# Kernel optimization log

Hardware: AMD Instinct MI355X
Metric: run time of the kernel (lower is better)

Reference implementation:

```python
import jax, jax.numpy as jnp
import numpy as np

N_NODES = 100000
N_EDGES = 600000
HIDDEN = 128
BN_EPS = 1e-5


def setup_inputs() -> dict:
    key = jax.random.key(0)
    k_x, k_e, k_w, k_b, k_g = jax.random.split(key, 5)
    x = jax.random.normal(k_x, (N_NODES, HIDDEN), dtype=jnp.float32)
    edge_index = jax.random.randint(k_e, (2, N_EDGES), 0, N_NODES, dtype=jnp.int64)
    # GCNConv linear weight (no bias on the linear; bias added post-aggregation)
    scale = 1.0 / np.sqrt(HIDDEN)
    W = jax.random.uniform(k_w, (HIDDEN, HIDDEN), jnp.float32, -scale, scale)
    b = jax.random.uniform(k_b, (HIDDEN,), jnp.float32, -scale, scale)
    gamma = jnp.ones((HIDDEN,), jnp.float32)   # BatchNorm weight
    beta = jnp.zeros((HIDDEN,), jnp.float32)   # BatchNorm bias
    return {"x": x, "edge_index": edge_index, "W": W, "b": b, "gamma": gamma, "beta": beta}


def reference(x, edge_index, W, b, gamma, beta):
    N = x.shape[0]
    # ReLU then GCNConv linear transform: [N, D]
    h = jnp.matmul(jax.nn.relu(x), W)
    # Add self-loops (PyG GCNConv default)
    loops = jnp.arange(N, dtype=edge_index.dtype)
    row = jnp.concatenate([edge_index[0], loops])  # source nodes
    col = jnp.concatenate([edge_index[1], loops])  # target nodes
    # Symmetric normalization deg^{-1/2} with unit edge weights
    ones = jnp.ones(row.shape[0], dtype=h.dtype)
    deg = jax.ops.segment_sum(ones, col, num_segments=N)
    dinv = jnp.where(deg > 0, jax.lax.rsqrt(deg), 0.0)
    norm = dinv[row] * dinv[col]  # [E+N]
    # Gather -> scale -> scatter-add aggregation, then conv bias
    agg = jax.ops.segment_sum(norm[:, None] * h[row], col, num_segments=N)
    out = agg + b
    # BatchNorm1d (training mode: batch stats, biased variance)
    mean = jnp.mean(out, axis=0)
    var = jnp.var(out, axis=0)
    return gamma * (out - mean) * jax.lax.rsqrt(var + BN_EPS) + beta
```

## Files before the change

kernel.cpp:

```cpp
#include <hip/hip_runtime.h>

#define D 128
#define CAP 32
#define BN_EPS 1e-5f

typedef float floatx4 __attribute__((ext_vector_type(4)));
typedef __bf16 bf16x8 __attribute__((ext_vector_type(8)));

__device__ inline unsigned short f2bf(float f) {
    unsigned u; __builtin_memcpy(&u, &f, 4);
    unsigned r = (u + 0x7FFFu + ((u >> 16) & 1u)) >> 16;
    return (unsigned short)r;
}
__device__ inline float bflo(unsigned v) { unsigned x = v << 16; float f; __builtin_memcpy(&f, &x, 4); return f; }
__device__ inline float bfhi(unsigned v) { unsigned x = v & 0xFFFF0000u; float f; __builtin_memcpy(&f, &x, 4); return f; }

__global__ void setup_k(const unsigned* __restrict__ e, int* __restrict__ flag,
                        int* __restrict__ cursor, float* __restrict__ sums,
                        float* __restrict__ sumsq, const float* __restrict__ W,
                        unsigned short* __restrict__ Wt, int n_nodes) {
    int i = blockIdx.x * blockDim.x + threadIdx.x;
    if (i < n_nodes) cursor[i] = 0;
    if (i < D) { sums[i] = 0.f; sumsq[i] = 0.f; }
    if (i < D * D) {
        int n = i >> 7, k = i & 127;
        Wt[n * D + k] = f2bf(W[k * D + n]);
    }
    if (i == 0) {
        unsigned acc = 0;
        for (int k = 0; k < 64; ++k) acc |= e[2 * k + 1];
        *flag = (acc == 0u) ? 1 : 0;
    }
}

__global__ __launch_bounds__(256, 2) void gb_k(const float* __restrict__ x,
                                               const unsigned short* __restrict__ Wt,
                                               unsigned short* __restrict__ h,
                                               int n_mtiles,
                                               const void* __restrict__ ep,
                                               const int* __restrict__ flag,
                                               int* __restrict__ cursor,
                                               int* __restrict__ bucket,
                                               int n_edges) {
    int b = blockIdx.x;
    int g = b >> 3;
    int ngroups = (int)gridDim.x >> 3;
    int nbg = ngroups >> 2;

    if ((g & 3) == 3) {
        int bb = (g >> 2) * 8 + (b & 7);
        int stride = nbg * 8 * 256;
        int fl = *flag;
        for (int e = bb * 256 + (int)threadIdx.x; e < n_edges; e += stride) {
            int r, c;
            if (fl) {
                const long long* p = (const long long*)ep;
                r = (int)p[e]; c = (int)p[e + n_edges];
            } else {
                const int* p = (const int*)ep;
                r = p[e]; c = p[e + n_edges];
            }
            int pos = atomicAdd(&cursor[c], 1);
            if (pos < CAP) bucket[(size_t)c * CAP + pos] = r;
        }
        return;
    }

    int gg = (g >> 2) * 3 + (g & 3);
    int gb = gg * 8 + (b & 7);
    int lane = threadIdx.x & 63;
    int wave = gb * 4 + (threadIdx.x >> 6);
    int nw = (ngroups - nbg) * 32;
    int l15 = lane & 15;
    int quad = lane >> 4;

    bf16x8 Bf[4][8];
    for (int ks = 0; ks < 4; ++ks)
        for (int j = 0; j < 8; ++j)
            Bf[ks][j] = *(const bf16x8*)(Wt + (size_t)(j * 16 + l15) * D + ks * 32 + quad * 8);

    for (int mt = wave; mt < n_mtiles; mt += nw) {
        const float* xrow = x + (size_t)(mt * 16 + l15) * D + quad * 8;
        bf16x8 Af[4];
        for (int ks = 0; ks < 4; ++ks) {
            float4 a0 = *(const float4*)(xrow + ks * 32);
            float4 a1 = *(const float4*)(xrow + ks * 32 + 4);
            float av[8] = {a0.x, a0.y, a0.z, a0.w, a1.x, a1.y, a1.z, a1.w};
            union { unsigned short u[8]; bf16x8 v; } tmp;
            for (int jj = 0; jj < 8; ++jj) tmp.u[jj] = f2bf(fmaxf(av[jj], 0.0f));
            Af[ks] = tmp.v;
        }
        floatx4 acc[8];
        for (int j = 0; j < 8; ++j) acc[j] = (floatx4){0.f, 0.f, 0.f, 0.f};
        for (int ks = 0; ks < 4; ++ks)
            for (int j = 0; j < 8; ++j)
                acc[j] = __builtin_amdgcn_mfma_f32_16x16x32_bf16(Af[ks], Bf[ks][j], acc[j], 0, 0, 0);
        for (int j = 0; j < 8; ++j)
            for (int reg = 0; reg < 4; ++reg) {
                int rr = mt * 16 + quad * 4 + reg;
                int cc = j * 16 + l15;
                h[(size_t)rr * D + cc] = f2bf(acc[j][reg]);
            }
    }
}

__global__ void dinv_k(const int* __restrict__ cursor, float* __restrict__ dinv, int n_nodes) {
    int i = blockIdx.x * blockDim.x + threadIdx.x;
    if (i < n_nodes) dinv[i] = rsqrtf(1.0f + (float)cursor[i]);
}

#define PREPD(s, rr) { int r_ = ((s) < degc) ? (rr) : node;              \
                       w##s = ((s) < degc) ? dinv[r_] : 0.0f;            \
                       hv##s = hp[(unsigned)r_ * 64u + lane]; }
#define ACC(s) { ax += w##s * bflo(hv##s); ay += w##s * bfhi(hv##s); }

__global__ __launch_bounds__(256) void agg_k(const unsigned short* __restrict__ h,
                                             const int* __restrict__ bucket,
                                             const int* __restrict__ cursor,
                                             const float* __restrict__ dinv,
                                             unsigned* __restrict__ aggb,
                                             int n_nodes) {
    int lane = threadIdx.x & 63;
    int node = blockIdx.x * 4 + (threadIdx.x >> 6);
    if (node >= n_nodes) return;
    const unsigned* hp = (const unsigned*)h;

    int deg = cursor[node];
    int degc = deg < CAP ? deg : CAP;
    float dc = dinv[node];

    unsigned v = hp[(unsigned)node * 64u + lane];
    float ax = dc * bflo(v), ay = dc * bfhi(v);
    const int* bk = bucket + (size_t)node * CAP;

    float w0=0,w1=0,w2=0,w3=0,w4=0,w5=0,w6=0,w7=0;
    unsigned hv0=0,hv1=0,hv2=0,hv3=0,hv4=0,hv5=0,hv6=0,hv7=0;

    if (degc > 0) { int4 b = *(const int4*)(bk);     PREPD(0,b.x) PREPD(1,b.y) PREPD(2,b.z) PREPD(3,b.w) }
    if (degc > 4) { int4 b = *(const int4*)(bk + 4); PREPD(4,b.x) PREPD(5,b.y) PREPD(6,b.z) PREPD(7,b.w) }

    if (degc <= 8) {
        ACC(0) ACC(1) ACC(2) ACC(3) ACC(4) ACC(5) ACC(6) ACC(7)
    } else {
        float w8=0,w9=0,w10=0,w11=0,w12=0,w13=0,w14=0,w15=0;
        unsigned hv8=0,hv9=0,hv10=0,hv11=0,hv12=0,hv13=0,hv14=0,hv15=0;
        { int4 b = *(const int4*)(bk + 8); PREPD(8,b.x) PREPD(9,b.y) PREPD(10,b.z) PREPD(11,b.w) }
        if (degc > 12) { int4 b = *(const int4*)(bk + 12); PREPD(12,b.x) PREPD(13,b.y) PREPD(14,b.z) PREPD(15,b.w) }
        ACC(0)  ACC(1)  ACC(2)  ACC(3)  ACC(4)  ACC(5)  ACC(6)  ACC(7)
        ACC(8)  ACC(9)  ACC(10) ACC(11) ACC(12) ACC(13) ACC(14) ACC(15)
        for (int e = 16; e < degc; ++e) {
            int r = bk[e];
            float dr = dinv[r];
            unsigned hh = hp[(unsigned)r * 64u + lane];
            ax += dr * bflo(hh); ay += dr * bfhi(hh);
        }
    }

    float ox = dc * ax, oy = dc * ay;
    aggb[(unsigned)node * 64u + lane] = ((unsigned)f2bf(oy) << 16) | (unsigned)f2bf(ox);
}

__global__ __launch_bounds__(256) void stats_k(const unsigned* __restrict__ aggb,
                                               float* __restrict__ sums, float* __restrict__ sumsq,
                                               int n_nodes) {
    __shared__ float red[256];
    int lane = threadIdx.x & 63;
    int wib = threadIdx.x >> 6;
    int wave = blockIdx.x * 4 + wib;
    int nw = gridDim.x * 4;
    float s0 = 0.f, s1 = 0.f, q0 = 0.f, q1 = 0.f;
    int n = wave;
    for (; n + 3 * nw < n_nodes; n += 4 * nw) {
        unsigned p0 = aggb[(size_t)n * 64 + lane];
        unsigned p1 = aggb[(size_t)(n + nw) * 64 + lane];
        unsigned p2 = aggb[(size_t)(n + 2 * nw) * 64 + lane];
        unsigned p3 = aggb[(size_t)(n + 3 * nw) * 64 + lane];
        float a0 = bflo(p0), b0 = bfhi(p0), a1 = bflo(p1), b1 = bfhi(p1);
        float a2 = bflo(p2), b2 = bfhi(p2), a3 = bflo(p3), b3 = bfhi(p3);
        s0 += a0 + a1 + a2 + a3;
        s1 += b0 + b1 + b2 + b3;
        q0 += a0 * a0 + a1 * a1 + a2 * a2 + a3 * a3;
        q1 += b0 * b0 + b1 * b1 + b2 * b2 + b3 * b3;
    }
    for (; n < n_nodes; n += nw) {
        unsigned p = aggb[(size_t)n * 64 + lane];
        float vx = bflo(p), vy = bfhi(p);
        s0 += vx; s1 += vy; q0 += vx * vx; q1 += vy * vy;
    }
    red[threadIdx.x] = s0; __syncthreads();
    if (wib == 0) atomicAdd(&sums[2 * lane], red[lane] + red[64 + lane] + red[128 + lane] + red[192 + lane]);
    __syncthreads();
    red[threadIdx.x] = s1; __syncthreads();
    if (wib == 0) atomicAdd(&sums[2 * lane + 1], red[lane] + red[64 + lane] + red[128 + lane] + red[192 + lane]);
    __syncthreads();
    red[threadIdx.x] = q0; __syncthreads();
    if (wib == 0) atomicAdd(&sumsq[2 * lane], red[lane] + red[64 + lane] + red[128 + lane] + red[192 + lane]);
    __syncthreads();
    red[threadIdx.x] = q1; __syncthreads();
    if (wib == 0) atomicAdd(&sumsq[2 * lane + 1], red[lane] + red[64 + lane] + red[128 + lane] + red[192 + lane]);
}

__global__ __launch_bounds__(256) void final_k(const unsigned* __restrict__ aggb,
                                               const float* __restrict__ sums, const float* __restrict__ sumsq,
                                               const float* __restrict__ gamma, const float* __restrict__ beta,
                                               float* __restrict__ out, int total4, float inv_n) {
    int i = blockIdx.x * blockDim.x + threadIdx.x;
    if (i >= total4) return;
    int idx = i * 4;
    int f = idx & (D - 1);
    float4 sm = *(const float4*)(sums + f);
    float4 sq = *(const float4*)(sumsq + f);
    float4 g  = *(const float4*)(gamma + f);
    float4 bt = *(const float4*)(beta + f);
    uint2 p = *(const uint2*)(aggb + i * 2);

    float m0 = sm.x * inv_n, m1 = sm.y * inv_n, m2 = sm.z * inv_n, m3 = sm.w * inv_n;
    float sc0 = g.x * rsqrtf(sq.x * inv_n - m0 * m0 + BN_EPS);
    float sc1 = g.y * rsqrtf(sq.y * inv_n - m1 * m1 + BN_EPS);
    float sc2 = g.z * rsqrtf(sq.z * inv_n - m2 * m2 + BN_EPS);
    float sc3 = g.w * rsqrtf(sq.w * inv_n - m3 * m3 + BN_EPS);
    float4 o;
    o.x = fmaf(bflo(p.x), sc0, bt.x - m0 * sc0);
    o.y = fmaf(bfhi(p.x), sc1, bt.y - m1 * sc1);
    o.z = fmaf(bflo(p.y), sc2, bt.z - m2 * sc2);
    o.w = fmaf(bfhi(p.y), sc3, bt.w - m3 * sc3);
    *(float4*)(out + idx) = o;
}

extern "C" void kernel_launch(void* const* d_in, const int* in_sizes, int n_in,
                              void* d_out, int out_size, void* d_ws, size_t ws_size,
                              hipStream_t stream) {
    const float* x     = (const float*)d_in[0];
    const void*  edges = d_in[1];
    const float* W     = (const float*)d_in[2];
    const float* gamma = (const float*)d_in[4];
    const float* beta  = (const float*)d_in[5];
    float* out = (float*)d_out;

    int N = in_sizes[0] / D;
    int E = in_sizes[1] / 2;

    char* ws = (char*)d_ws;
    size_t off = 0;
    auto alloc = [&](size_t bytes) { void* p = ws + off; off += (bytes + 255) & ~(size_t)255; return p; };
    unsigned short* h  = (unsigned short*)alloc((size_t)N * D * 2);
    unsigned* aggb     = (unsigned*)alloc((size_t)N * D * 2);
    int* bucket        = (int*)alloc((size_t)N * CAP * 4);
    int* cursor        = (int*)alloc((size_t)N * 4);
    float* dinv        = (float*)alloc((size_t)N * 4);
    unsigned short* Wt = (unsigned short*)alloc((size_t)D * D * 2);
    float* sums        = (float*)alloc(512);
    float* sumsq       = (float*)alloc(512);
    int* flag          = (int*)alloc(16);

    int nblk = (N + 255) / 256;
    int n_mtiles = N / 16;

    setup_k<<<nblk, 256, 0, stream>>>((const unsigned*)edges, flag, cursor, sums, sumsq, W, Wt, N);
    gb_k<<<2080, 256, 0, stream>>>(x, Wt, h, n_mtiles, edges, flag, cursor, bucket, E);
    dinv_k<<<nblk, 256, 0, stream>>>(cursor, dinv, N);
    agg_k<<<(N + 3) / 4, 256, 0, stream>>>(h, bucket, cursor, dinv, aggb, N);
    stats_k<<<512, 256, 0, stream>>>(aggb, sums, sumsq, N);
    final_k<<<(N * D / 4 + 255) / 256, 256, 0, stream>>>(aggb, sums, sumsq, gamma, beta, out, N * D / 4, 1.0f / (float)N);
}
```

Measured before the change: 230.2 us.

## Co-schedule bucketing wave inside every GEMM block with unrolled batched atomics

Instead of assigning one quarter of the block groups to edge bucketing, each block now devotes one of its four waves (rotating by block index) to bucketing while the other three do the bf16 MFMA GEMM. The bucketing loop is unrolled twelve-fold, issuing all loads, then all atomics, then all stores, to expose memory-level parallelism. The int64 path reads only the low 32-bit word, and the grid shrinks from 2080 to 1024 blocks. This aims to overlap the latency-bound atomic scatter with the compute-bound GEMM on every CU, at the cost of more registers per thread and an imbalance if one role finishes much earlier than the other.

```diff
diff --git a/kernel.cpp b/kernel.cpp
--- a/kernel.cpp
+++ b/kernel.cpp
@@ -43,34 +43,47 @@
                                                int* __restrict__ bucket,
                                                int n_edges) {
     int b = blockIdx.x;
-    int g = b >> 3;
-    int ngroups = (int)gridDim.x >> 3;
-    int nbg = ngroups >> 2;
-
-    if ((g & 3) == 3) {
-        int bb = (g >> 2) * 8 + (b & 7);
-        int stride = nbg * 8 * 256;
+    int wib = threadIdx.x >> 6;
+    int lane = threadIdx.x & 63;
+    int bwsel = b & 3;
+
+    if (wib == bwsel) {
+        const int UN = 12;
         int fl = *flag;
-        for (int e = bb * 256 + (int)threadIdx.x; e < n_edges; e += stride) {
-            int r, c;
-            if (fl) {
-                const long long* p = (const long long*)ep;
-                r = (int)p[e]; c = (int)p[e + n_edges];
-            } else {
-                const int* p = (const int*)ep;
-                r = p[e]; c = p[e + n_edges];
-            }
-            int pos = atomicAdd(&cursor[c], 1);
-            if (pos < CAP) bucket[(size_t)c * CAP + pos] = r;
+        int base = b * (UN * 64);
+        int stride = (int)gridDim.x * (UN * 64);
+        for (int e0 = base; e0 < n_edges; e0 += stride) {
+            int r[UN], c[UN], pos[UN];
+#pragma unroll
+            for (int k = 0; k < UN; ++k) {
+                int e = e0 + k * 64 + lane;
+                bool ok = e < n_edges;
+                if (fl) {
+                    const int* p = (const int*)ep;
+                    r[k] = ok ? p[2 * e] : 0;
+                    c[k] = ok ? p[2 * (e + n_edges)] : 0;
+                } else {
+                    const int* p = (const int*)ep;
+                    r[k] = ok ? p[e] : 0;
+                    c[k] = ok ? p[e + n_edges] : 0;
+                }
+            }
+#pragma unroll
+            for (int k = 0; k < UN; ++k) {
+                int e = e0 + k * 64 + lane;
+                pos[k] = (e < n_edges) ? atomicAdd(&cursor[c[k]], 1) : CAP;
+            }
+#pragma unroll
+            for (int k = 0; k < UN; ++k) {
+                if (pos[k] < CAP) bucket[(size_t)c[k] * CAP + pos[k]] = r[k];
+            }
         }
         return;
     }
 
-    int gg = (g >> 2) * 3 + (g & 3);
-    int gb = gg * 8 + (b & 7);
-    int lane = threadIdx.x & 63;
-    int wave = gb * 4 + (threadIdx.x >> 6);
-    int nw = (ngroups - nbg) * 32;
+    int gw = wib - (wib > bwsel ? 1 : 0);
+    int wave = b * 3 + gw;
+    int nw = (int)gridDim.x * 3;
     int l15 = lane & 15;
     int quad = lane >> 4;
 
@@ -257,7 +270,7 @@
     int n_mtiles = N / 16;
 
     setup_k<<<nblk, 256, 0, stream>>>((const unsigned*)edges, flag, cursor, sums, sumsq, W, Wt, N);
-    gb_k<<<2080, 256, 0, stream>>>(x, Wt, h, n_mtiles, edges, flag, cursor, bucket, E);
+    gb_k<<<1024, 256, 0, stream>>>(x, Wt, h, n_mtiles, edges, flag, cursor, bucket, E);
     dinv_k<<<nblk, 256, 0, stream>>>(cursor, dinv, N);
     agg_k<<<(N + 3) / 4, 256, 0, stream>>>(h, bucket, cursor, dinv, aggb, N);
     stats_k<<<512, 256, 0, stream>>>(aggb, sums, sumsq, N);
```

After: 234.8 us. Within noise of the previous version (+2.0%).

## Fuse dinv into aggregation, unroll bucket fill, put bucket blocks first

Applied to the files above, without the earlier changes.

Removes the separate dinv kernel and its buffer, computing rsqrt(1+deg) on the fly from cursor inside the aggregation kernel. The bucket-fill loop now handles two edges per iteration so two atomics are in flight at once, and the bucket blocks become a contiguous leading range of 512 blocks instead of being interleaved among the GEMM blocks. The aim is to save a launch and a pass over memory, at the cost of extra rsqrt work in the gather path. Placing bucket blocks first changes how the atomic-heavy and MFMA work overlap.

```diff
diff --git a/kernel.cpp b/kernel.cpp
--- a/kernel.cpp
+++ b/kernel.cpp
@@ -41,24 +41,39 @@
                                                const int* __restrict__ flag,
                                                int* __restrict__ cursor,
                                                int* __restrict__ bucket,
-                                               int n_edges) {
+                                               int n_edges, int n_bb) {
     int b = blockIdx.x;
-    int g = b >> 3;
-    int ngroups = (int)gridDim.x >> 3;
-    int nbg = ngroups >> 2;
-
-    if ((g & 3) == 3) {
-        int bb = (g >> 2) * 8 + (b & 7);
-        int stride = nbg * 8 * 256;
+    int lane = threadIdx.x & 63;
+
+    if (b < n_bb) {
+        int tid = b * 256 + (int)threadIdx.x;
+        int nt = n_bb * 256;
         int fl = *flag;
-        for (int e = bb * 256 + (int)threadIdx.x; e < n_edges; e += stride) {
+        int e0 = tid, e1 = tid + nt;
+        for (; e1 < n_edges; e0 += 2 * nt, e1 += 2 * nt) {
+            int r0, c0, r1, c1;
+            if (fl) {
+                const long long* p = (const long long*)ep;
+                r0 = (int)p[e0]; c0 = (int)p[e0 + n_edges];
+                r1 = (int)p[e1]; c1 = (int)p[e1 + n_edges];
+            } else {
+                const int* p = (const int*)ep;
+                r0 = p[e0]; c0 = p[e0 + n_edges];
+                r1 = p[e1]; c1 = p[e1 + n_edges];
+            }
+            int p0 = atomicAdd(&cursor[c0], 1);
+            int p1 = atomicAdd(&cursor[c1], 1);
+            if (p0 < CAP) bucket[(size_t)c0 * CAP + p0] = r0;
+            if (p1 < CAP) bucket[(size_t)c1 * CAP + p1] = r1;
+        }
+        for (; e0 < n_edges; e0 += nt) {
             int r, c;
             if (fl) {
                 const long long* p = (const long long*)ep;
-                r = (int)p[e]; c = (int)p[e + n_edges];
+                r = (int)p[e0]; c = (int)p[e0 + n_edges];
             } else {
                 const int* p = (const int*)ep;
-                r = p[e]; c = p[e + n_edges];
+                r = p[e0]; c = p[e0 + n_edges];
             }
             int pos = atomicAdd(&cursor[c], 1);
             if (pos < CAP) bucket[(size_t)c * CAP + pos] = r;
@@ -66,11 +81,9 @@
         return;
     }
 
-    int gg = (g >> 2) * 3 + (g & 3);
-    int gb = gg * 8 + (b & 7);
-    int lane = threadIdx.x & 63;
-    int wave = gb * 4 + (threadIdx.x >> 6);
-    int nw = (ngroups - nbg) * 32;
+    int gbi = b - n_bb;
+    int wave = gbi * 4 + (threadIdx.x >> 6);
+    int nw = ((int)gridDim.x - n_bb) * 4;
     int l15 = lane & 15;
     int quad = lane >> 4;
 
@@ -104,20 +117,15 @@
     }
 }
 
-__global__ void dinv_k(const int* __restrict__ cursor, float* __restrict__ dinv, int n_nodes) {
-    int i = blockIdx.x * blockDim.x + threadIdx.x;
-    if (i < n_nodes) dinv[i] = rsqrtf(1.0f + (float)cursor[i]);
-}
-
-#define PREPD(s, rr) { int r_ = ((s) < degc) ? (rr) : node;              \
-                       w##s = ((s) < degc) ? dinv[r_] : 0.0f;            \
+#define PREPD(s, rr) { int r_ = ((s) < degc) ? (rr) : node;                        \
+                       int d_ = cursor[r_];                                         \
+                       w##s = ((s) < degc) ? rsqrtf(1.0f + (float)d_) : 0.0f;       \
                        hv##s = hp[(unsigned)r_ * 64u + lane]; }
 #define ACC(s) { ax += w##s * bflo(hv##s); ay += w##s * bfhi(hv##s); }
 
 __global__ __launch_bounds__(256) void agg_k(const unsigned short* __restrict__ h,
                                              const int* __restrict__ bucket,
                                              const int* __restrict__ cursor,
-                                             const float* __restrict__ dinv,
                                              unsigned* __restrict__ aggb,
                                              int n_nodes) {
     int lane = threadIdx.x & 63;
@@ -127,7 +135,7 @@
 
     int deg = cursor[node];
     int degc = deg < CAP ? deg : CAP;
-    float dc = dinv[node];
+    float dc = rsqrtf(1.0f + (float)deg);
 
     unsigned v = hp[(unsigned)node * 64u + lane];
     float ax = dc * bflo(v), ay = dc * bfhi(v);
@@ -150,7 +158,7 @@
         ACC(8)  ACC(9)  ACC(10) ACC(11) ACC(12) ACC(13) ACC(14) ACC(15)
         for (int e = 16; e < degc; ++e) {
             int r = bk[e];
-            float dr = dinv[r];
+            float dr = rsqrtf(1.0f + (float)cursor[r]);
             unsigned hh = hp[(unsigned)r * 64u + lane];
             ax += dr * bflo(hh); ay += dr * bfhi(hh);
         }
@@ -247,7 +255,6 @@
     unsigned* aggb     = (unsigned*)alloc((size_t)N * D * 2);
     int* bucket        = (int*)alloc((size_t)N * CAP * 4);
     int* cursor        = (int*)alloc((size_t)N * 4);
-    float* dinv        = (float*)alloc((size_t)N * 4);
     unsigned short* Wt = (unsigned short*)alloc((size_t)D * D * 2);
     float* sums        = (float*)alloc(512);
     float* sumsq       = (float*)alloc(512);
@@ -257,9 +264,8 @@
     int n_mtiles = N / 16;
 
     setup_k<<<nblk, 256, 0, stream>>>((const unsigned*)edges, flag, cursor, sums, sumsq, W, Wt, N);
-    gb_k<<<2080, 256, 0, stream>>>(x, Wt, h, n_mtiles, edges, flag, cursor, bucket, E);
-    dinv_k<<<nblk, 256, 0, stream>>>(cursor, dinv, N);
-    agg_k<<<(N + 3) / 4, 256, 0, stream>>>(h, bucket, cursor, dinv, aggb, N);
+    gb_k<<<2080, 256, 0, stream>>>(x, Wt, h, n_mtiles, edges, flag, cursor, bucket, E, 512);
+    agg_k<<<(N + 3) / 4, 256, 0, stream>>>(h, bucket, cursor, aggb, N);
     stats_k<<<512, 256, 0, stream>>>(aggb, sums, sumsq, N);
     final_k<<<(N * D / 4 + 255) / 256, 256, 0, stream>>>(aggb, sums, sumsq, gamma, beta, out, N * D / 4, 1.0f / (float)N);
 }
```

New measurement: 269.5 us. 1.17x slower.
